# Optimization experiments

Hardware: AMD Instinct MI355X
Metric: run time of the kernel (lower is better)

## Reference

```python
import jax, jax.numpy as jnp
import numpy as np

N = 3072          # num nodes
H = 256           # hidden_features
B = 4             # num_heads
HD = H // B       # per-head dim
PRIOR_MU = 1.0
PRIOR_SIGMA = 1.0
LN_EPS = 1e-5


def setup_inputs() -> dict:
    key = jax.random.key(0)
    ks = jax.random.split(key, 12)
    s = 0.02  # weight init scale
    return {
        "h": jax.random.normal(ks[0], (N, H), jnp.float32),
        "gamma": jnp.ones((H,), jnp.float32),
        "beta": jnp.zeros((H,), jnp.float32),
        "W_k": jax.random.normal(ks[1], (H, H), jnp.float32) * s,
        "b_k": jnp.zeros((H,), jnp.float32),
        "W_mu": jax.random.normal(ks[2], (H, H), jnp.float32) * s,
        "b_mu": jnp.zeros((H,), jnp.float32),
        "W_ls": jax.random.normal(ks[3], (H, H), jnp.float32) * s,
        "b_ls": jnp.zeros((H,), jnp.float32),
        "W_v": jax.random.normal(ks[4], (H * B, H), jnp.float32) * s,
        "b_v": jnp.zeros((H,), jnp.float32),
        "diffusion": jax.random.uniform(ks[5], (N, N, 1), jnp.float32),
        "eps": jax.random.normal(ks[6], (N, N, B), jnp.float32),
    }


def reference(h, gamma, beta, W_k, b_k, W_mu, b_mu, W_ls, b_ls, W_v, b_v, diffusion, eps):
    h0 = h
    # LayerNorm
    mean = jnp.mean(h, axis=-1, keepdims=True)
    var = jnp.var(h, axis=-1, keepdims=True)
    hn = (h - mean) * jax.lax.rsqrt(var + LN_EPS) * gamma + beta
    # Q/K-style projections, split into heads: [N, HD, B]
    k = (hn @ W_k + b_k).reshape(N, HD, B)
    mu = (hn @ W_mu + b_mu).reshape(N, HD, B)
    ls = (hn @ W_ls + b_ls).reshape(N, HD, B)
    scale = HD ** -0.5
    mu = jnp.einsum('xyb,zyb->xzb', k, mu) * scale       # [N, N, B]
    ls = jnp.einsum('xyb,zyb->xzb', k, ls) * scale       # [N, N, B]
    sigma = jax.nn.softplus(ls)
    # KL(LogNormal(mu, sigma) || LogNormal(log(prior_mu), prior_sigma))
    mu_p = jnp.log(jnp.asarray(PRIOR_MU, h.dtype))
    sig_p = jnp.asarray(PRIOR_SIGMA, h.dtype)
    kl = (jnp.log(sig_p / sigma)
          + (sigma ** 2 + (mu - mu_p) ** 2) / (2.0 * sig_p ** 2)
          - 0.5)
    kl = (kl * jnp.sign(diffusion)).sum(-1).mean()
    # reparameterized LogNormal sample, masked by diffusion matrix
    a = jnp.exp(mu + sigma * eps) * diffusion            # [N, N, B]
    # L1 normalize over source-node axis (dim=-2), torch F.normalize semantics
    denom = jnp.clip(jnp.sum(jnp.abs(a), axis=-2, keepdims=True), 1e-12)
    a = a / denom
    # diffusion-weighted aggregation: [N, B, H] -> [N, B*H]
    out = jnp.einsum('xyb,yz->xbz', a, hn).reshape(N, B * H)
    out = out @ W_v + b_v                                 # fc_v (dropout = eval mode)
    out = jax.nn.elu(out) + h0
    return out, kl
```

## Files before the change

kernel.cpp:

```cpp
#include <hip/hip_runtime.h>
#include <hip/hip_bf16.h>


#define NN 3072
#define HH 256
#define NB 4
#define HD 64
constexpr int KS = 2;
constexpr int CZ = 256;
constexpr int NCH = NN / CZ;
constexpr int KMLSZ = 192 * 2 * 64 * 8;

typedef __attribute__((ext_vector_type(8))) short bf16x8;
typedef __attribute__((ext_vector_type(4))) float f32x4;

static __device__ inline short f2bf(float f) {
    __hip_bfloat16 h = __float2bfloat16(f);
    return __builtin_bit_cast(short, h);
}

typedef const __attribute__((address_space(1))) unsigned int* gas_ptr;
typedef __attribute__((address_space(3))) unsigned int* las_ptr;
static __device__ inline void gload_lds16(const void* g, void* l) {
    __builtin_amdgcn_global_load_lds((gas_ptr)g, (las_ptr)l, 16, 0, 0);
}

__global__ void k0_prep(const float* __restrict__ Wk, const float* __restrict__ Wmu,
                        const float* __restrict__ Wls, const float* __restrict__ bk,
                        const float* __restrict__ bmu, const float* __restrict__ bls,
                        const float* __restrict__ Wv, short* __restrict__ WTcat,
                        float* __restrict__ biascat, short* __restrict__ WvT,
                        float* __restrict__ denom) {
    __shared__ float t[64][65];
    int bx = blockIdx.x;
    if (bx < 48) {
        int mat = bx >> 4;
        int by = (bx >> 2) & 3, bc = bx & 3;
        int y0 = by * 64, c0 = bc * 64;
        const float* W = (mat == 0) ? Wk : (mat == 1 ? Wmu : Wls);
        float scale = (mat == 0) ? 0.125f : 1.f;
        int r = threadIdx.x >> 4, c4 = (threadIdx.x & 15) * 4;
#pragma unroll
        for (int i = 0; i < 4; i++) {
            int yl = r + i * 16;
            float4 v = *(const float4*)(W + (y0 + yl) * 256 + c0 + c4);
            t[yl][c4] = v.x; t[yl][c4 + 1] = v.y; t[yl][c4 + 2] = v.z; t[yl][c4 + 3] = v.w;
        }
        __syncthreads();
#pragma unroll
        for (int i = 0; i < 4; i++) {
            int cl = r + i * 16;
            int corig = c0 + cl;
            int cp = mat * 256 + (corig & 3) * 64 + (corig >> 2);
            short4 v = make_short4(f2bf(t[c4][cl] * scale), f2bf(t[c4 + 1][cl] * scale),
                                   f2bf(t[c4 + 2][cl] * scale), f2bf(t[c4 + 3][cl] * scale));
            *(short4*)(WTcat + cp * 256 + y0 + c4) = v;
        }
        return;
    }
    if (bx < 112) {
        int b = bx - 48;
        int bk2 = b >> 2, bn = b & 3;
        int k0 = bk2 * 64, n0 = bn * 64;
        int r = threadIdx.x >> 4, c4 = (threadIdx.x & 15) * 4;
#pragma unroll
        for (int i = 0; i < 4; i++) {
            int kk = r + i * 16;
            float4 v = *(const float4*)(Wv + (k0 + kk) * 256 + n0 + c4);
            t[kk][c4] = v.x; t[kk][c4 + 1] = v.y; t[kk][c4 + 2] = v.z; t[kk][c4 + 3] = v.w;
        }
        __syncthreads();
#pragma unroll
        for (int i = 0; i < 4; i++) {
            int nn = r + i * 16;
            short4 v = make_short4(f2bf(t[c4][nn]), f2bf(t[c4 + 1][nn]),
                                   f2bf(t[c4 + 2][nn]), f2bf(t[c4 + 3][nn]));
            *(short4*)(WvT + (n0 + nn) * 1024 + k0 + c4) = v;
        }
        return;
    }
    if (bx == 112) {
        int cc = threadIdx.x;
        int corig = (cc & 63) * 4 + (cc >> 6);
        biascat[cc] = bk[corig] * 0.125f;
        biascat[256 + cc] = bmu[corig];
        biascat[512 + cc] = bls[corig];
        return;
    }
    int i = (bx - 113) * 256 + threadIdx.x;
    if (i < 13312) denom[i] = 0.f;
}

__global__ void k1_ln(const float* __restrict__ h, const float* __restrict__ gamma,
                      const float* __restrict__ beta, short* __restrict__ hn) {
    int row = blockIdx.x, tid = threadIdx.x;
    float v = h[row * 256 + tid];
    float s = v, s2 = v * v;
    for (int off = 32; off; off >>= 1) {
        s += __shfl_xor(s, off);
        s2 += __shfl_xor(s2, off);
    }
    __shared__ float red[8];
    int w = tid >> 6, lane = tid & 63;
    if (!lane) { red[w] = s; red[4 + w] = s2; }
    __syncthreads();
    s = red[0] + red[1] + red[2] + red[3];
    s2 = red[4] + red[5] + red[6] + red[7];
    float mean = s * (1.f / 256.f);
    float var = s2 * (1.f / 256.f) - mean * mean;
    float rs = rsqrtf(var + 1e-5f);
    hn[row * 256 + tid] = f2bf((v - mean) * rs * gamma[tid] + beta[tid]);
}

__global__ void k1b_tr(const short* __restrict__ hn, short* __restrict__ hnT) {
    __shared__ short t[64][68];
    int bn = blockIdx.x >> 2, bh = blockIdx.x & 3;
    int n0 = bn * 64, h0 = bh * 64;
    int r = threadIdx.x >> 4, c4 = (threadIdx.x & 15) * 4;
#pragma unroll
    for (int i = 0; i < 4; i++) {
        int nn = r + i * 16;
        *(short4*)&t[nn][c4] = *(const short4*)(hn + (n0 + nn) * 256 + h0 + c4);
    }
    __syncthreads();
#pragma unroll
    for (int i = 0; i < 4; i++) {
        int hh = r + i * 16;
        short4 v = make_short4(t[c4][hh], t[c4 + 1][hh], t[c4 + 2][hh], t[c4 + 3][hh]);
        *(short4*)(hnT + (h0 + hh) * NN + n0 + c4) = v;
    }
}

__global__ __launch_bounds__(256) void k2_proj(const short* __restrict__ hn,
                                               const short* __restrict__ WTcat,
                                               const float* __restrict__ biascat,
                                               short* __restrict__ kml) {
    int bx = blockIdx.x;
    int mt = bx / 12, nb = bx % 12;
    int m0 = mt * 64, n0 = nb * 64;
    int tid = threadIdx.x, w = tid >> 6, lane = tid & 63, q = lane >> 4, c = lane & 15;
    int mrow = m0 + w * 16;
    f32x4 acc[4] = {{0, 0, 0, 0}, {0, 0, 0, 0}, {0, 0, 0, 0}, {0, 0, 0, 0}};
    for (int k0 = 0; k0 < 256; k0 += 32) {
        bf16x8 af = *(const bf16x8*)(hn + (mrow + c) * 256 + k0 + q * 8);
#pragma unroll
        for (int nt = 0; nt < 4; nt++) {
            bf16x8 bf = *(const bf16x8*)(WTcat + (n0 + nt * 16 + c) * 256 + k0 + q * 8);
            acc[nt] = __builtin_amdgcn_mfma_f32_16x16x32_bf16(af, bf, acc[nt], 0, 0, 0);
        }
    }
#pragma unroll
    for (int nt = 0; nt < 4; nt++) {
        int cp = n0 + nt * 16 + c;
        float bias = biascat[cp];
        int mat = cp >> 8, b = (cp >> 6) & 3, y = cp & 63;
        short* dst = kml + (size_t)(mat * 4 + b) * KMLSZ;
        int kh2 = y >> 5, lq = (y >> 3) & 3, j = y & 7;
        int zt = mt * 4 + w;
#pragma unroll
        for (int r = 0; r < 4; r++) {
            int ml = 4 * q + r;
            dst[(((zt * 2 + kh2) * 64) + lq * 16 + ml) * 8 + j] = f2bf(acc[nt][r] + bias);
        }
    }
}

__global__ __launch_bounds__(256) void k3a_elem(
    const short* __restrict__ kml, const float* __restrict__ eps,
    const float* __restrict__ diff, short* __restrict__ a,
    float* __restrict__ denom, float* __restrict__ klsum) {
    __shared__ float klred[4];
    const int tid = threadIdx.x;
    const int w = tid >> 6, lane = tid & 63, q = lane >> 4, c = lane & 15;
    const int xt = blockIdx.x % 192;
    const int ch = blockIdx.x / 192;
    const int x0 = xt * 16;
    const int zw = ch * CZ + w * 64;

    bf16x8 qf[NB][2];
#pragma unroll
    for (int b = 0; b < NB; b++)
#pragma unroll
        for (int kh = 0; kh < 2; kh++)
            qf[b][kh] = *(const bf16x8*)(kml + (size_t)b * KMLSZ +
                                         ((xt * 2 + kh) * 64 + lane) * 8);

    float den_acc[NB] = {0.f, 0.f, 0.f, 0.f};
    float kl_acc = 0.f;
    const size_t xrow = (size_t)(x0 + c) * NN;

#pragma unroll
    for (int t = 0; t < 4; t++) {
        const int z = zw + t * 16;
        const int zt2 = z >> 4;
        f32x4 e4[4];
        float dif[4];
#pragma unroll
        for (int r = 0; r < 4; r++) {
            e4[r] = *(const f32x4*)(eps + (xrow + (size_t)(z + 4 * q + r)) * 4);
            dif[r] = diff[xrow + z + 4 * q + r];
        }
#pragma unroll
        for (int b = 0; b < NB; b++) {
            const short* mup = kml + (size_t)(NB + b) * KMLSZ;
            const short* lsp = kml + (size_t)(2 * NB + b) * KMLSZ;
            bf16x8 a0 = *(const bf16x8*)(mup + ((zt2 * 2 + 0) * 64 + lane) * 8);
            bf16x8 a1 = *(const bf16x8*)(mup + ((zt2 * 2 + 1) * 64 + lane) * 8);
            f32x4 smu = {0.f, 0.f, 0.f, 0.f};
            smu = __builtin_amdgcn_mfma_f32_16x16x32_bf16(a0, qf[b][0], smu, 0, 0, 0);
            smu = __builtin_amdgcn_mfma_f32_16x16x32_bf16(a1, qf[b][1], smu, 0, 0, 0);
            bf16x8 l0 = *(const bf16x8*)(lsp + ((zt2 * 2 + 0) * 64 + lane) * 8);
            bf16x8 l1 = *(const bf16x8*)(lsp + ((zt2 * 2 + 1) * 64 + lane) * 8);
            f32x4 sls = {0.f, 0.f, 0.f, 0.f};
            sls = __builtin_amdgcn_mfma_f32_16x16x32_bf16(l0, qf[b][0], sls, 0, 0, 0);
            sls = __builtin_amdgcn_mfma_f32_16x16x32_bf16(l1, qf[b][1], sls, 0, 0, 0);
            short pk[4];
#pragma unroll
            for (int r = 0; r < 4; r++) {
                float mu = smu[r];
                float ls = sls[r];
                float e = e4[r][b];
                float d = dif[r];
                float ex = __expf(-fabsf(ls));
                float sg = fmaxf(ls, 0.f) + __logf(1.f + ex);
                float kle = -__logf(sg) + 0.5f * (sg * sg + mu * mu) - 0.5f;
                float sgn = (d > 0.f) ? 1.f : ((d < 0.f) ? -1.f : 0.f);
                kl_acc += sgn * kle;
                float av = __expf(mu + sg * e) * d;
                den_acc[b] += fabsf(av);
                pk[r] = f2bf(av);
            }
            *(short4*)(a + ((size_t)b * NN + x0 + c) * NN + z + 4 * q) =
                make_short4(pk[0], pk[1], pk[2], pk[3]);
        }
    }
#pragma unroll
    for (int b = 0; b < NB; b++) {
        float d = den_acc[b];
        d += __shfl_down(d, 32);
        d += __shfl_down(d, 16);
        if (q == 0) atomicAdd(&denom[(x0 + c) * NB + b], d);
    }
    for (int off = 32; off; off >>= 1) kl_acc += __shfl_xor(kl_acc, off);
    if (lane == 0) klred[w] = kl_acc;
    __syncthreads();
    if (tid == 0) atomicAdd(klsum, klred[0] + klred[1] + klred[2] + klred[3]);
}

__global__ __launch_bounds__(256) void k3b_agg(
    const short* __restrict__ a, const short* __restrict__ hnT,
    float* __restrict__ aggp) {
    __shared__ short As[2][64 * 64];
    __shared__ short Bs[2][256 * 64];
    const int tid = threadIdx.x;
    const int w = tid >> 6, lane = tid & 63, q = lane >> 4, c = lane & 15;
    const int bid = blockIdx.x;
    const int b = bid & 3;
    const int ksp = (bid >> 2) & 1;
    const int m0 = (bid >> 3) * 64;
    const int kbase = ksp * (NN / KS);

    const char* Ag = (const char*)(a + ((size_t)b * NN + m0) * NN + kbase);
    const char* Bg = (const char*)(hnT + kbase);

    f32x4 acc[4][4];
#pragma unroll
    for (int i = 0; i < 4; i++)
#pragma unroll
        for (int j = 0; j < 4; j++) acc[i][j] = (f32x4){0.f, 0.f, 0.f, 0.f};

    auto stage = [&](int buf, int ks) {
        const int kb = ks * 128;
#pragma unroll
        for (int l = 0; l < 2; l++) {
            int idx = l * 256 + tid;
            int row = idx >> 3;
            int colb = ((idx & 7) * 16) ^ ((row & 7) << 4);
            gload_lds16(Ag + (size_t)row * (NN * 2) + kb + colb,
                        (char*)&As[buf][0] + idx * 16);
        }
#pragma unroll
        for (int l = 0; l < 8; l++) {
            int idx = l * 256 + tid;
            int row = idx >> 3;
            int colb = ((idx & 7) * 16) ^ ((row & 7) << 4);
            gload_lds16(Bg + (size_t)row * (NN * 2) + kb + colb,
                        (char*)&Bs[buf][0] + idx * 16);
        }
    };

    stage(0, 0);
    int cur = 0;
    for (int ks = 0; ks < NN / KS / 64; ks++) {
        __syncthreads();
        if (ks + 1 < NN / KS / 64) stage(cur ^ 1, ks + 1);
        bf16x8 af[4][2], bf[4][2];
#pragma unroll
        for (int mt = 0; mt < 4; mt++) {
            int row = mt * 16 + c;
#pragma unroll
            for (int kh = 0; kh < 2; kh++) {
                int col = (kh * 64 + q * 16) ^ ((row & 7) << 4);
                af[mt][kh] = *(const bf16x8*)((const char*)&As[cur][0] + row * 128 + col);
            }
        }
#pragma unroll
        for (int nt = 0; nt < 4; nt++) {
            int row = w * 64 + nt * 16 + c;
#pragma unroll
            for (int kh = 0; kh < 2; kh++) {
                int col = (kh * 64 + q * 16) ^ ((row & 7) << 4);
                bf[nt][kh] = *(const bf16x8*)((const char*)&Bs[cur][0] + row * 128 + col);
            }
        }
#pragma unroll
        for (int mt = 0; mt < 4; mt++)
#pragma unroll
            for (int nt = 0; nt < 4; nt++) {
                acc[mt][nt] = __builtin_amdgcn_mfma_f32_16x16x32_bf16(
                    af[mt][0], bf[nt][0], acc[mt][nt], 0, 0, 0);
                acc[mt][nt] = __builtin_amdgcn_mfma_f32_16x16x32_bf16(
                    af[mt][1], bf[nt][1], acc[mt][nt], 0, 0, 0);
            }
        cur ^= 1;
    }

    float* dst = aggp + (size_t)ksp * (NN * NB * HH);
#pragma unroll
    for (int mt = 0; mt < 4; mt++)
#pragma unroll
        for (int nt = 0; nt < 4; nt++)
#pragma unroll
            for (int r = 0; r < 4; r++) {
                int x = m0 + mt * 16 + 4 * q + r;
                int n = w * 64 + nt * 16 + c;
                dst[(size_t)x * 1024 + b * 256 + n] = acc[mt][nt][r];
            }
}

__global__ void k35_norm(const float* __restrict__ aggp, const float* __restrict__ denom,
                         short* __restrict__ aggn) {
    int x = blockIdx.x, tid = threadIdx.x;
    int b = tid >> 6;
    int h4 = (tid & 63) * 4;
    size_t base = ((size_t)x * 4 + b) * 256 + h4;
    float4 s = {0.f, 0.f, 0.f, 0.f};
#pragma unroll
    for (int sp = 0; sp < KS; sp++) {
        float4 v = *(const float4*)(aggp + (size_t)sp * (NN * 4 * 256) + base);
        s.x += v.x; s.y += v.y; s.z += v.z; s.w += v.w;
    }
    float r = 1.f / fmaxf(denom[x * 4 + b], 1e-12f);
    short4 o = make_short4(f2bf(s.x * r), f2bf(s.y * r), f2bf(s.z * r), f2bf(s.w * r));
    *(short4*)(aggn + base) = o;
}

__global__ __launch_bounds__(256) void k4_out(const short* __restrict__ aggn,
                                              const short* __restrict__ WvT,
                                              const float* __restrict__ bv,
                                              const float* __restrict__ h,
                                              const float* __restrict__ klsum,
                                              float* __restrict__ out) {
    int bx = blockIdx.x;
    int mt = bx >> 2, nb = bx & 3;
    int m0 = mt * 64, n0 = nb * 64;
    int tid = threadIdx.x, w = tid >> 6, lane = tid & 63, q = lane >> 4, c = lane & 15;
    int mrow = m0 + w * 16;
    f32x4 acc[4] = {{0, 0, 0, 0}, {0, 0, 0, 0}, {0, 0, 0, 0}, {0, 0, 0, 0}};
    for (int k0 = 0; k0 < 1024; k0 += 32) {
        bf16x8 af = *(const bf16x8*)(aggn + (mrow + c) * 1024 + k0 + q * 8);
#pragma unroll
        for (int nt = 0; nt < 4; nt++) {
            bf16x8 bf = *(const bf16x8*)(WvT + (n0 + nt * 16 + c) * 1024 + k0 + q * 8);
            acc[nt] = __builtin_amdgcn_mfma_f32_16x16x32_bf16(af, bf, acc[nt], 0, 0, 0);
        }
    }
#pragma unroll
    for (int nt = 0; nt < 4; nt++) {
        int col = n0 + nt * 16 + c;
        float bias = bv[col];
#pragma unroll
        for (int r = 0; r < 4; r++) {
            int row = mrow + 4 * q + r;
            float v = acc[nt][r] + bias;
            v = (v > 0.f) ? v : (__expf(v) - 1.f);
            out[row * 256 + col] = v + h[row * 256 + col];
        }
    }
    if (bx == 0 && tid == 0) out[786432] = klsum[0] * (1.0f / 9437184.0f);
}

extern "C" void kernel_launch(void* const* d_in, const int* in_sizes, int n_in,
                              void* d_out, int out_size, void* d_ws, size_t ws_size,
                              hipStream_t stream) {
    const float* h = (const float*)d_in[0];
    const float* gamma = (const float*)d_in[1];
    const float* beta = (const float*)d_in[2];
    const float* Wk = (const float*)d_in[3];
    const float* bk = (const float*)d_in[4];
    const float* Wmu = (const float*)d_in[5];
    const float* bmu = (const float*)d_in[6];
    const float* Wls = (const float*)d_in[7];
    const float* bls = (const float*)d_in[8];
    const float* Wv = (const float*)d_in[9];
    const float* bv = (const float*)d_in[10];
    const float* diff = (const float*)d_in[11];
    const float* eps = (const float*)d_in[12];
    float* out = (float*)d_out;

    char* p = (char*)d_ws;
    short* a = (short*)p;      p += (size_t)75497472;
    float* aggp = (float*)p;   p += (size_t)KS * 12582912;
    float* denom = (float*)p;  p += 49152;
    float* klsum = (float*)p;  p += 4096;
    short* hn = (short*)p;     p += 1572864;
    short* hnT = (short*)p;    p += 1572864;
    short* kml = (short*)p;    p += 4718592;
    short* WTcat = (short*)p;  p += 393216;
    float* biasc = (float*)p;  p += 4096;
    short* WvT = (short*)p;    p += 524288;
    short* aggn = (short*)p;

    k0_prep<<<165, 256, 0, stream>>>(Wk, Wmu, Wls, bk, bmu, bls, Wv, WTcat, biasc, WvT,
                                     denom);
    k1_ln<<<3072, 256, 0, stream>>>(h, gamma, beta, hn);
    k1b_tr<<<192, 256, 0, stream>>>(hn, hnT);
    k2_proj<<<576, 256, 0, stream>>>(hn, WTcat, biasc, kml);
    k3a_elem<<<192 * NCH, 256, 0, stream>>>(kml, eps, diff, a, denom, klsum);
    k3b_agg<<<48 * NB * KS, 256, 0, stream>>>(a, hnT, aggp);
    k35_norm<<<3072, 256, 0, stream>>>(aggp, denom, aggn);
    k4_out<<<192, 256, 0, stream>>>(aggn, WvT, bv, h, klsum, out);
}
```

Before: 437.4 us.

## Store attention weights in MFMA fragment layout and fuse normalization into aggregation

```diff
diff --git a/kernel.cpp b/kernel.cpp
--- a/kernel.cpp
+++ b/kernel.cpp
@@ -6,9 +6,6 @@
 #define HH 256
 #define NB 4
 #define HD 64
-constexpr int KS = 2;
-constexpr int CZ = 256;
-constexpr int NCH = NN / CZ;
 constexpr int KMLSZ = 192 * 2 * 64 * 8;
 
 typedef __attribute__((ext_vector_type(8))) short bf16x8;
@@ -167,15 +164,26 @@
 
 __global__ __launch_bounds__(256) void k3a_elem(
     const short* __restrict__ kml, const float* __restrict__ eps,
-    const float* __restrict__ diff, short* __restrict__ a,
+    const float* __restrict__ diff, short* __restrict__ apk,
     float* __restrict__ denom, float* __restrict__ klsum) {
+    __shared__ short frag[2][16][512];
     __shared__ float klred[4];
     const int tid = threadIdx.x;
     const int w = tid >> 6, lane = tid & 63, q = lane >> 4, c = lane & 15;
-    const int xt = blockIdx.x % 192;
-    const int ch = blockIdx.x / 192;
+    const int xb = blockIdx.x % 48;
+    const int zc = blockIdx.x / 48;
+    const int xt = xb * 4 + w;
     const int x0 = xt * 16;
-    const int zw = ch * CZ + w * 64;
+
+    auto stage = [&](int buf, int zt2) {
+#pragma unroll
+        for (int i = 0; i < 4; i++) {
+            int f = w * 4 + i;
+            int mat = f >> 3, bh = (f >> 1) & 3, kh = f & 1;
+            const short* plane = kml + (size_t)((mat + 1) * 4 + bh) * KMLSZ;
+            gload_lds16(plane + ((zt2 * 2 + kh) * 64 + lane) * 8, &frag[buf][f][0]);
+        }
+    };
 
     bf16x8 qf[NB][2];
 #pragma unroll
@@ -185,32 +193,34 @@
             qf[b][kh] = *(const bf16x8*)(kml + (size_t)b * KMLSZ +
                                          ((xt * 2 + kh) * 64 + lane) * 8);
 
+    stage(0, zc * 4);
+
     float den_acc[NB] = {0.f, 0.f, 0.f, 0.f};
     float kl_acc = 0.f;
     const size_t xrow = (size_t)(x0 + c) * NN;
 
-#pragma unroll
     for (int t = 0; t < 4; t++) {
-        const int z = zw + t * 16;
-        const int zt2 = z >> 4;
+        const int buf = t & 1;
+        const int zt2 = zc * 4 + t;
+        const int z16 = zt2 * 16;
+        __syncthreads();
+        if (t < 3) stage(buf ^ 1, zt2 + 1);
         f32x4 e4[4];
         float dif[4];
 #pragma unroll
         for (int r = 0; r < 4; r++) {
-            e4[r] = *(const f32x4*)(eps + (xrow + (size_t)(z + 4 * q + r)) * 4);
-            dif[r] = diff[xrow + z + 4 * q + r];
+            e4[r] = *(const f32x4*)(eps + (xrow + (size_t)(z16 + 4 * q + r)) * 4);
+            dif[r] = diff[xrow + z16 + 4 * q + r];
         }
 #pragma unroll
         for (int b = 0; b < NB; b++) {
-            const short* mup = kml + (size_t)(NB + b) * KMLSZ;
-            const short* lsp = kml + (size_t)(2 * NB + b) * KMLSZ;
-            bf16x8 a0 = *(const bf16x8*)(mup + ((zt2 * 2 + 0) * 64 + lane) * 8);
-            bf16x8 a1 = *(const bf16x8*)(mup + ((zt2 * 2 + 1) * 64 + lane) * 8);
+            bf16x8 a0 = *(const bf16x8*)&frag[buf][b * 2 + 0][lane * 8];
+            bf16x8 a1 = *(const bf16x8*)&frag[buf][b * 2 + 1][lane * 8];
+            bf16x8 l0 = *(const bf16x8*)&frag[buf][8 + b * 2 + 0][lane * 8];
+            bf16x8 l1 = *(const bf16x8*)&frag[buf][8 + b * 2 + 1][lane * 8];
             f32x4 smu = {0.f, 0.f, 0.f, 0.f};
             smu = __builtin_amdgcn_mfma_f32_16x16x32_bf16(a0, qf[b][0], smu, 0, 0, 0);
             smu = __builtin_amdgcn_mfma_f32_16x16x32_bf16(a1, qf[b][1], smu, 0, 0, 0);
-            bf16x8 l0 = *(const bf16x8*)(lsp + ((zt2 * 2 + 0) * 64 + lane) * 8);
-            bf16x8 l1 = *(const bf16x8*)(lsp + ((zt2 * 2 + 1) * 64 + lane) * 8);
             f32x4 sls = {0.f, 0.f, 0.f, 0.f};
             sls = __builtin_amdgcn_mfma_f32_16x16x32_bf16(l0, qf[b][0], sls, 0, 0, 0);
             sls = __builtin_amdgcn_mfma_f32_16x16x32_bf16(l1, qf[b][1], sls, 0, 0, 0);
@@ -230,7 +240,7 @@
                 den_acc[b] += fabsf(av);
                 pk[r] = f2bf(av);
             }
-            *(short4*)(a + ((size_t)b * NN + x0 + c) * NN + z + 4 * q) =
+            *(short4*)(apk + (((size_t)b * 192 + xt) * 192 + zt2) * 256 + c * 16 + q * 4) =
                 make_short4(pk[0], pk[1], pk[2], pk[3]);
         }
     }
@@ -248,111 +258,70 @@
 }
 
 __global__ __launch_bounds__(256) void k3b_agg(
-    const short* __restrict__ a, const short* __restrict__ hnT,
-    float* __restrict__ aggp) {
-    __shared__ short As[2][64 * 64];
-    __shared__ short Bs[2][256 * 64];
+    const short* __restrict__ apk, const short* __restrict__ hnT,
+    const float* __restrict__ denom, short* __restrict__ aggn) {
+    __shared__ float red[2][64 * 33];
     const int tid = threadIdx.x;
     const int w = tid >> 6, lane = tid & 63, q = lane >> 4, c = lane & 15;
+    const int kw = w >> 1, nw = w & 1;
     const int bid = blockIdx.x;
     const int b = bid & 3;
-    const int ksp = (bid >> 2) & 1;
-    const int m0 = (bid >> 3) * 64;
-    const int kbase = ksp * (NN / KS);
-
-    const char* Ag = (const char*)(a + ((size_t)b * NN + m0) * NN + kbase);
-    const char* Bg = (const char*)(hnT + kbase);
-
-    f32x4 acc[4][4];
+    const int nb = (bid >> 2) & 3;
+    const int mb = bid >> 4;
+    const int m0 = mb * 64;
+    const int n0 = nb * 64 + nw * 32;
+    const int q2 = q >> 1, q1 = q & 1;
+
+    f32x4 acc[4][2];
 #pragma unroll
     for (int i = 0; i < 4; i++)
 #pragma unroll
-        for (int j = 0; j < 4; j++) acc[i][j] = (f32x4){0.f, 0.f, 0.f, 0.f};
-
-    auto stage = [&](int buf, int ks) {
-        const int kb = ks * 128;
-#pragma unroll
-        for (int l = 0; l < 2; l++) {
-            int idx = l * 256 + tid;
-            int row = idx >> 3;
-            int colb = ((idx & 7) * 16) ^ ((row & 7) << 4);
-            gload_lds16(Ag + (size_t)row * (NN * 2) + kb + colb,
-                        (char*)&As[buf][0] + idx * 16);
-        }
-#pragma unroll
-        for (int l = 0; l < 8; l++) {
-            int idx = l * 256 + tid;
-            int row = idx >> 3;
-            int colb = ((idx & 7) * 16) ^ ((row & 7) << 4);
-            gload_lds16(Bg + (size_t)row * (NN * 2) + kb + colb,
-                        (char*)&Bs[buf][0] + idx * 16);
-        }
-    };
-
-    stage(0, 0);
-    int cur = 0;
-    for (int ks = 0; ks < NN / KS / 64; ks++) {
-        __syncthreads();
-        if (ks + 1 < NN / KS / 64) stage(cur ^ 1, ks + 1);
-        bf16x8 af[4][2], bf[4][2];
-#pragma unroll
-        for (int mt = 0; mt < 4; mt++) {
-            int row = mt * 16 + c;
-#pragma unroll
-            for (int kh = 0; kh < 2; kh++) {
-                int col = (kh * 64 + q * 16) ^ ((row & 7) << 4);
-                af[mt][kh] = *(const bf16x8*)((const char*)&As[cur][0] + row * 128 + col);
-            }
-        }
-#pragma unroll
-        for (int nt = 0; nt < 4; nt++) {
-            int row = w * 64 + nt * 16 + c;
-#pragma unroll
-            for (int kh = 0; kh < 2; kh++) {
-                int col = (kh * 64 + q * 16) ^ ((row & 7) << 4);
-                bf[nt][kh] = *(const bf16x8*)((const char*)&Bs[cur][0] + row * 128 + col);
-            }
-        }
+        for (int j = 0; j < 2; j++) acc[i][j] = (f32x4){0.f, 0.f, 0.f, 0.f};
+
+    const size_t abase = ((size_t)b * 192 + mb * 4) * 192 * 256;
+    for (int ks = 0; ks < 48; ks++) {
+        const int kglob = kw * 1536 + ks * 32;
+        const int T2 = kw * 96 + ks * 2;
+        bf16x8 af[4], bf[2];
 #pragma unroll
         for (int mt = 0; mt < 4; mt++)
-#pragma unroll
-            for (int nt = 0; nt < 4; nt++) {
+            af[mt] = *(const bf16x8*)(apk + abase +
+                                      (size_t)(mt * 192 + T2 + q2) * 256 + c * 16 + q1 * 8);
+#pragma unroll
+        for (int nt = 0; nt < 2; nt++)
+            bf[nt] = *(const bf16x8*)(hnT + (size_t)(n0 + nt * 16 + c) * NN + kglob + q * 8);
+#pragma unroll
+        for (int mt = 0; mt < 4; mt++)
+#pragma unroll
+            for (int nt = 0; nt < 2; nt++)
                 acc[mt][nt] = __builtin_amdgcn_mfma_f32_16x16x32_bf16(
-                    af[mt][0], bf[nt][0], acc[mt][nt], 0, 0, 0);
-                acc[mt][nt] = __builtin_amdgcn_mfma_f32_16x16x32_bf16(
-                    af[mt][1], bf[nt][1], acc[mt][nt], 0, 0, 0);
-            }
-        cur ^= 1;
-    }
-
-    float* dst = aggp + (size_t)ksp * (NN * NB * HH);
-#pragma unroll
-    for (int mt = 0; mt < 4; mt++)
-#pragma unroll
-        for (int nt = 0; nt < 4; nt++)
+                    af[mt], bf[nt], acc[mt][nt], 0, 0, 0);
+    }
+
+    if (kw == 1) {
+#pragma unroll
+        for (int mt = 0; mt < 4; mt++)
+#pragma unroll
+            for (int nt = 0; nt < 2; nt++)
+#pragma unroll
+                for (int r = 0; r < 4; r++)
+                    red[nw][(mt * 16 + 4 * q + r) * 33 + nt * 16 + c] = acc[mt][nt][r];
+    }
+    __syncthreads();
+    if (kw == 0) {
+#pragma unroll
+        for (int mt = 0; mt < 4; mt++)
 #pragma unroll
             for (int r = 0; r < 4; r++) {
                 int x = m0 + mt * 16 + 4 * q + r;
-                int n = w * 64 + nt * 16 + c;
-                dst[(size_t)x * 1024 + b * 256 + n] = acc[mt][nt][r];
+                float rcp = 1.f / fmaxf(denom[x * 4 + b], 1e-12f);
+#pragma unroll
+                for (int nt = 0; nt < 2; nt++) {
+                    float s = acc[mt][nt][r] + red[nw][(mt * 16 + 4 * q + r) * 33 + nt * 16 + c];
+                    aggn[(size_t)x * 1024 + b * 256 + n0 + nt * 16 + c] = f2bf(s * rcp);
+                }
             }
-}
-
-__global__ void k35_norm(const float* __restrict__ aggp, const float* __restrict__ denom,
-                         short* __restrict__ aggn) {
-    int x = blockIdx.x, tid = threadIdx.x;
-    int b = tid >> 6;
-    int h4 = (tid & 63) * 4;
-    size_t base = ((size_t)x * 4 + b) * 256 + h4;
-    float4 s = {0.f, 0.f, 0.f, 0.f};
-#pragma unroll
-    for (int sp = 0; sp < KS; sp++) {
-        float4 v = *(const float4*)(aggp + (size_t)sp * (NN * 4 * 256) + base);
-        s.x += v.x; s.y += v.y; s.z += v.z; s.w += v.w;
-    }
-    float r = 1.f / fmaxf(denom[x * 4 + b], 1e-12f);
-    short4 o = make_short4(f2bf(s.x * r), f2bf(s.y * r), f2bf(s.z * r), f2bf(s.w * r));
-    *(short4*)(aggn + base) = o;
+    }
 }
 
 __global__ __launch_bounds__(256) void k4_out(const short* __restrict__ aggn,
@@ -409,8 +378,7 @@
     float* out = (float*)d_out;
 
     char* p = (char*)d_ws;
-    short* a = (short*)p;      p += (size_t)75497472;
-    float* aggp = (float*)p;   p += (size_t)KS * 12582912;
+    short* apk = (short*)p;    p += (size_t)75497472;
     float* denom = (float*)p;  p += 49152;
     float* klsum = (float*)p;  p += 4096;
     short* hn = (short*)p;     p += 1572864;
@@ -418,7 +386,8 @@
     short* kml = (short*)p;    p += 4718592;
     short* WTcat = (short*)p;  p += 393216;
     float* biasc = (float*)p;  p += 4096;
-    short* WvT = (short*)p;    p += 524288;
+    short* WvT = (short*)p;
+    p += 524288;
     short* aggn = (short*)p;
 
     k0_prep<<<165, 256, 0, stream>>>(Wk, Wmu, Wls, bk, bmu, bls, Wv, WTcat, biasc, WvT,
@@ -426,8 +395,7 @@
     k1_ln<<<3072, 256, 0, stream>>>(h, gamma, beta, hn);
     k1b_tr<<<192, 256, 0, stream>>>(hn, hnT);
     k2_proj<<<576, 256, 0, stream>>>(hn, WTcat, biasc, kml);
-    k3a_elem<<<192 * NCH, 256, 0, stream>>>(kml, eps, diff, a, denom, klsum);
-    k3b_agg<<<48 * NB * KS, 256, 0, stream>>>(a, hnT, aggp);
-    k35_norm<<<3072, 256, 0, stream>>>(aggp, denom, aggn);
+    k3a_elem<<<48 * 48, 256, 0, stream>>>(kml, eps, diff, apk, denom, klsum);
+    k3b_agg<<<48 * 4 * 4, 256, 0, stream>>>(apk, hnT, denom, aggn);
     k4_out<<<192, 256, 0, stream>>>(aggn, WvT, bv, h, klsum, out);
 }
```

Result: no change. 433.9 us (-0.8%).
